# Optimization experiments

Hardware: AMD Instinct MI355X
Metric: run time of the kernel (lower is better)

The kernel has to match this reference:

```python
import jax, jax.numpy as jnp
import numpy as np

B = 131072      # batch of states
STATE = 32      # state dim
HIDDEN = 256    # MLP hidden width
NOUT = 32       # MLP outputs (summed after relu -> scalar value)
ACT = 8         # action dim (QP size)
QP_ITERS = 30   # BoxCDQP coordinate-descent sweeps


def setup_inputs() -> dict:
    key = jax.random.key(0)
    ks = jax.random.split(key, 8)
    sc = lambda fan: 1.0 / np.sqrt(fan)
    x = jax.random.normal(ks[0], (B, STATE), jnp.float32)
    t = jnp.zeros((1,), jnp.float32)
    W0 = jax.random.normal(ks[1], (STATE, HIDDEN), jnp.float32) * sc(STATE)
    b0 = jnp.zeros((HIDDEN,), jnp.float32)
    W1 = jax.random.normal(ks[2], (HIDDEN, HIDDEN), jnp.float32) * sc(HIDDEN)
    b1 = jnp.zeros((HIDDEN,), jnp.float32)
    W2 = jax.random.normal(ks[3], (HIDDEN, HIDDEN), jnp.float32) * sc(HIDDEN)
    b2 = jnp.zeros((HIDDEN,), jnp.float32)
    Wout = jax.random.normal(ks[4], (HIDDEN, NOUT), jnp.float32) * sc(HIDDEN)
    bout = jnp.zeros((NOUT,), jnp.float32)
    G = jax.random.normal(ks[5], (STATE, ACT), jnp.float32) * sc(STATE)
    A = jax.random.normal(ks[6], (ACT, ACT), jnp.float32)
    R = A @ A.T / ACT + jnp.eye(ACT, dtype=jnp.float32)  # symmetric PD cost
    lower = -jnp.ones((ACT,), jnp.float32)
    upper = jnp.ones((ACT,), jnp.float32)
    return dict(x=x, t=t, W0=W0, b0=b0, W1=W1, b1=b1, W2=W2, b2=b2,
                Wout=Wout, bout=bout, G=G, R=R, lower=lower, upper=upper)


def _v(xi, W0, b0, W1, b1, W2, b2, Wout, bout):
    # v(x) = sum(relu(MLP(angle_rep(x)))), angle_rep = identity here
    h = jax.nn.softplus(xi @ W0 + b0)
    h = jax.nn.softplus(h @ W1 + b1)
    h = jax.nn.softplus(h @ W2 + b2)
    return jnp.sum(jax.nn.relu(h @ Wout + bout))


def _box_cdqp(Q, c, lo, hi):
    # BoxCDQP: min 0.5 u^T Q u + c^T u  s.t. lo <= u <= hi, cyclic coord descent
    diag = jnp.diag(Q)

    def sweep(u, _):
        for i in range(ACT):  # ACT is small and static -> unrolled
            gi = Q[i] @ u + c[i]
            u = u.at[i].set(jnp.clip(u[i] - gi / diag[i], lo[i], hi[i]))
        return u, None

    u, _ = jax.lax.scan(sweep, jnp.zeros_like(c), None, length=QP_ITERS)
    return u


def reference(x, t, W0, b0, W1, b1, W2, b2, Wout, bout, G, R, lower, upper):
    # dv/dx per sample via grad of scalar v, batched with vmap
    dvdx = jax.vmap(
        lambda xi: jax.grad(_v)(xi, W0, b0, W1, b1, W2, b2, Wout, bout)
    )(x)                                  # [B, STATE]
    c = dvdx @ G                          # [B, ACT] linear QP term (dvdx @ gx)
    Q = 2.0 * R                           # params_obj = (2*R, dvdx_gx)
    u = jax.vmap(lambda ci: _box_cdqp(Q, ci, lower, upper))(c)  # [B, ACT]
    return u
```

## Files before the change

kernel.cpp:

```cpp
#include <hip/hip_runtime.h>
#include <math.h>

typedef float f4 __attribute__((ext_vector_type(4)));

#define THREADS 256
#define HID 256
#define SMP 16
#define CH 16

__global__ void k_prep(const float* __restrict__ W1, const float* __restrict__ W2,
                       const float* __restrict__ Wout, float* __restrict__ ws) {
  float* W1T = ws;
  float* W2T = ws + 65536;
  float* WoutT = ws + 131072;
  int tid = blockIdx.x * 256 + threadIdx.x;
  if (tid < 65536) {
    int k = tid >> 8, n = tid & 255;
    W1T[tid] = W1[n * 256 + k];
    W2T[tid] = W2[n * 256 + k];
    if (tid < 8192) {
      int k2 = tid >> 8, n2 = tid & 255;
      WoutT[tid] = Wout[n2 * 32 + k2];
    }
  }
}

__device__ __forceinline__ float sp_cr(float z) {
  float az = fabsf(z);
  float e  = (float)exp(-(double)az);
  float lp = (float)log1p((double)e);
  return fmaxf(z, 0.0f) + lp;
}

__device__ __forceinline__ float sig_from_h(float h) {
  return 1.0f - __expf(-h);
}

__device__ __forceinline__ void mac_fwd4(const float* __restrict__ h0r,
                                         const float* __restrict__ h1r,
                                         const float* __restrict__ h2r,
                                         const float* __restrict__ h3r,
                                         const float* __restrict__ wl,
                                         int l, f4& a0, f4& a1, f4& a2, f4& a3) {
#pragma clang fp contract(off)
  #pragma unroll
  for (int k = 0; k < CH; k += 4) {
    f4 x0 = *(const f4*)&h0r[k];
    f4 x1 = *(const f4*)&h1r[k];
    f4 x2 = *(const f4*)&h2r[k];
    f4 x3 = *(const f4*)&h3r[k];
    #pragma unroll
    for (int kk = 0; kk < 4; ++kk) {
      f4 wv = *(const f4*)&wl[(k + kk) * 256 + l * 4];
      #pragma unroll
      for (int m = 0; m < 4; ++m) { float p = x0[kk] * wv[m]; a0[m] = a0[m] + p; }
      #pragma unroll
      for (int m = 0; m < 4; ++m) { float p = x1[kk] * wv[m]; a1[m] = a1[m] + p; }
      #pragma unroll
      for (int m = 0; m < 4; ++m) { float p = x2[kk] * wv[m]; a2[m] = a2[m] + p; }
      #pragma unroll
      for (int m = 0; m < 4; ++m) { float p = x3[kk] * wv[m]; a3[m] = a3[m] + p; }
    }
  }
}

__device__ __forceinline__ void mac_bwd4(const float* __restrict__ h0r,
                                         const float* __restrict__ h1r,
                                         const float* __restrict__ h2r,
                                         const float* __restrict__ h3r,
                                         const float* __restrict__ wl,
                                         int l, f4& a0, f4& a1, f4& a2, f4& a3) {
  #pragma unroll
  for (int k = 0; k < CH; k += 4) {
    f4 x0 = *(const f4*)&h0r[k];
    f4 x1 = *(const f4*)&h1r[k];
    f4 x2 = *(const f4*)&h2r[k];
    f4 x3 = *(const f4*)&h3r[k];
    #pragma unroll
    for (int kk = 0; kk < 4; ++kk) {
      f4 wv = *(const f4*)&wl[(k + kk) * 256 + l * 4];
      #pragma unroll
      for (int m = 0; m < 4; ++m) a0[m] = fmaf(x0[kk], wv[m], a0[m]);
      #pragma unroll
      for (int m = 0; m < 4; ++m) a1[m] = fmaf(x1[kk], wv[m], a1[m]);
      #pragma unroll
      for (int m = 0; m < 4; ++m) a2[m] = fmaf(x2[kk], wv[m], a2[m]);
      #pragma unroll
      for (int m = 0; m < 4; ++m) a3[m] = fmaf(x3[kk], wv[m], a3[m]);
    }
  }
}

template <int K, bool FWD>
__device__ __forceinline__ void staged_layer(
    const float* __restrict__ Wbase,
    const float* __restrict__ hin,
    int sA, int l, int tid, f4* wbuf4, const float* wl,
    f4& a0, f4& a1, f4& a2, f4& a3) {
  a0 = (f4){0, 0, 0, 0}; a1 = a0; a2 = a0; a3 = a0;
  const f4* src = (const f4*)Wbase;
  f4 r0 = src[tid];
  f4 r1 = src[tid + THREADS];
  f4 r2 = src[tid + 2 * THREADS];
  f4 r3 = src[tid + 3 * THREADS];
  constexpr int NC = K / CH;
  #pragma unroll 1
  for (int c = 0; c < NC; ++c) {
    __syncthreads();
    wbuf4[tid] = r0;
    wbuf4[tid + THREADS] = r1;
    wbuf4[tid + 2 * THREADS] = r2;
    wbuf4[tid + 3 * THREADS] = r3;
    __syncthreads();
    if (c + 1 < NC) {
      const f4* s2 = (const f4*)(Wbase + (size_t)(c + 1) * CH * 256);
      r0 = s2[tid];
      r1 = s2[tid + THREADS];
      r2 = s2[tid + 2 * THREADS];
      r3 = s2[tid + 3 * THREADS];
    }
    const float* h0 = hin + (size_t)(sA + 0) * K + c * CH;
    const float* h1 = hin + (size_t)(sA + 1) * K + c * CH;
    const float* h2 = hin + (size_t)(sA + 2) * K + c * CH;
    const float* h3 = hin + (size_t)(sA + 3) * K + c * CH;
    if constexpr (FWD) mac_fwd4(h0, h1, h2, h3, wl, l, a0, a1, a2, a3);
    else               mac_bwd4(h0, h1, h2, h3, wl, l, a0, a1, a2, a3);
  }
}

__device__ __forceinline__ void sp_store(f4 a, const float* __restrict__ b,
                                         float* __restrict__ dstrow, int l) {
  f4 bv = *(const f4*)&b[l * 4];
  f4 o;
  #pragma unroll
  for (int m = 0; m < 4; ++m) o[m] = sp_cr(a[m] + bv[m]);
  *(f4*)&dstrow[l * 4] = o;
}

__device__ __forceinline__ void sig_store(f4 a, float* __restrict__ hrow, int l) {
  f4 h = *(f4*)&hrow[l * 4];
  #pragma unroll
  for (int m = 0; m < 4; ++m) h[m] = a[m] * sig_from_h(h[m]);
  *(f4*)&hrow[l * 4] = h;
}

__global__ __launch_bounds__(THREADS, 2) void k_main(
    const float* __restrict__ x,
    const float* __restrict__ W0, const float* __restrict__ b0,
    const float* __restrict__ W1, const float* __restrict__ b1,
    const float* __restrict__ W2, const float* __restrict__ b2,
    const float* __restrict__ Wout, const float* __restrict__ bout,
    const float* __restrict__ G, const float* __restrict__ ws,
    float* __restrict__ out) {
  __shared__ float xs[SMP][32];
  __shared__ float ha[SMP][HID];
  __shared__ float hb[SMP][HID];
  __shared__ float hc[SMP][HID];
  __shared__ float zm[SMP][32];
  __shared__ f4 wbuf4[CH * 64];
  float* wl = (float*)wbuf4;

  const float* W1T = ws;
  const float* W2T = ws + 65536;
  const float* WoutT = ws + 131072;

  const int tid = threadIdx.x;
  const int w = tid >> 6;
  const int l = tid & 63;
  const int sA = w * 4;
  const int s0 = blockIdx.x * SMP;

  for (int i = tid; i < SMP * 32; i += THREADS) {
    xs[i >> 5][i & 31] = x[(size_t)s0 * 32 + i];
  }

  {
    f4 a0, a1, a2, a3;
    staged_layer<32, true>(W0, &xs[0][0], sA, l, tid, wbuf4, wl, a0, a1, a2, a3);
    sp_store(a0, b0, &ha[sA + 0][0], l);
    sp_store(a1, b0, &ha[sA + 1][0], l);
    sp_store(a2, b0, &ha[sA + 2][0], l);
    sp_store(a3, b0, &ha[sA + 3][0], l);
  }

  {
    f4 a0, a1, a2, a3;
    staged_layer<256, true>(W1, &ha[0][0], sA, l, tid, wbuf4, wl, a0, a1, a2, a3);
    sp_store(a0, b1, &hb[sA + 0][0], l);
    sp_store(a1, b1, &hb[sA + 1][0], l);
    sp_store(a2, b1, &hb[sA + 2][0], l);
    sp_store(a3, b1, &hb[sA + 3][0], l);
  }

  {
    f4 a0, a1, a2, a3;
    staged_layer<256, true>(W2, &hb[0][0], sA, l, tid, wbuf4, wl, a0, a1, a2, a3);
    sp_store(a0, b2, &hc[sA + 0][0], l);
    sp_store(a1, b2, &hc[sA + 1][0], l);
    sp_store(a2, b2, &hc[sA + 2][0], l);
    sp_store(a3, b2, &hc[sA + 3][0], l);
  }
  __syncthreads();

  {
#pragma clang fp contract(off)
    #pragma unroll
    for (int rep = 0; rep < 2; ++rep) {
      int idx = tid + rep * THREADS;
      int s = idx >> 5, j = idx & 31;
      const float* wrow = WoutT + (size_t)j * 256;
      float acc = 0.0f;
      #pragma unroll 4
      for (int k = 0; k < 256; k += 4) {
        f4 hv = *(const f4*)&hc[s][k];
        f4 wv = *(const f4*)&wrow[k];
        #pragma unroll
        for (int kk = 0; kk < 4; ++kk) {
          float p = hv[kk] * wv[kk];
          acc = acc + p;
        }
      }
      zm[s][j] = (acc + bout[j] > 0.0f) ? 1.0f : 0.0f;
    }
  }

  {
    f4 a0, a1, a2, a3;
    staged_layer<32, false>(WoutT, &zm[0][0], sA, l, tid, wbuf4, wl, a0, a1, a2, a3);
    sig_store(a0, &hc[sA + 0][0], l);
    sig_store(a1, &hc[sA + 1][0], l);
    sig_store(a2, &hc[sA + 2][0], l);
    sig_store(a3, &hc[sA + 3][0], l);
  }

  {
    f4 a0, a1, a2, a3;
    staged_layer<256, false>(W2T, &hc[0][0], sA, l, tid, wbuf4, wl, a0, a1, a2, a3);
    sig_store(a0, &hb[sA + 0][0], l);
    sig_store(a1, &hb[sA + 1][0], l);
    sig_store(a2, &hb[sA + 2][0], l);
    sig_store(a3, &hb[sA + 3][0], l);
  }

  {
    f4 a0, a1, a2, a3;
    staged_layer<256, false>(W1T, &hb[0][0], sA, l, tid, wbuf4, wl, a0, a1, a2, a3);
    sig_store(a0, &ha[sA + 0][0], l);
    sig_store(a1, &ha[sA + 1][0], l);
    sig_store(a2, &ha[sA + 2][0], l);
    sig_store(a3, &ha[sA + 3][0], l);
  }
  __syncthreads();

  {
    #pragma unroll
    for (int rep = 0; rep < 2; ++rep) {
      int idx = tid + rep * THREADS;
      int s = idx >> 5, j = idx & 31;
      const float* wrow = W0 + (size_t)j * 256;
      float acc = 0.0f;
      #pragma unroll 4
      for (int k = 0; k < 256; k += 4) {
        f4 hv = *(const f4*)&ha[s][k];
        f4 wv = *(const f4*)&wrow[k];
        #pragma unroll
        for (int kk = 0; kk < 4; ++kk) {
          acc = fmaf(hv[kk], wv[kk], acc);
        }
      }
      zm[s][j] = acc;
    }
  }
  __syncthreads();

  if (tid < SMP * 8) {
    int s = tid >> 3, a = tid & 7;
    float acc = 0.0f;
    #pragma unroll
    for (int j = 0; j < 32; ++j) acc = fmaf(zm[s][j], G[j * 8 + a], acc);
    out[(size_t)(s0 + s) * 8 + a] = acc;
  }
}

__global__ __launch_bounds__(256) void k_qp(float* __restrict__ out,
                                            const float* __restrict__ R,
                                            const float* __restrict__ lower,
                                            const float* __restrict__ upper) {
  int t = blockIdx.x * 256 + threadIdx.x;
  float q[8][8], u[8], cc[8], lo[8], hi[8], dg[8];
  #pragma unroll
  for (int i = 0; i < 8; ++i) {
    lo[i] = lower[i];
    hi[i] = upper[i];
    u[i] = 0.0f;
    cc[i] = out[(size_t)t * 8 + i];
    #pragma unroll
    for (int j = 0; j < 8; ++j) q[i][j] = 2.0f * R[i * 8 + j];
  }
  #pragma unroll
  for (int i = 0; i < 8; ++i) dg[i] = q[i][i];

  #pragma unroll 1
  for (int it = 0; it < 30; ++it) {
    #pragma unroll
    for (int i = 0; i < 8; ++i) {
      float g = cc[i];
      #pragma unroll
      for (int j = 0; j < 8; ++j) g = fmaf(q[i][j], u[j], g);
      float v = u[i] - g / dg[i];
      u[i] = fminf(fmaxf(v, lo[i]), hi[i]);
    }
  }
  #pragma unroll
  for (int i = 0; i < 8; ++i) out[(size_t)t * 8 + i] = u[i];
}

extern "C" void kernel_launch(void* const* d_in, const int* in_sizes, int n_in,
                              void* d_out, int out_size, void* d_ws, size_t ws_size,
                              hipStream_t stream) {
  const float* x    = (const float*)d_in[0];
  const float* W0   = (const float*)d_in[2];
  const float* b0   = (const float*)d_in[3];
  const float* W1   = (const float*)d_in[4];
  const float* b1   = (const float*)d_in[5];
  const float* W2   = (const float*)d_in[6];
  const float* b2   = (const float*)d_in[7];
  const float* Wout = (const float*)d_in[8];
  const float* bout = (const float*)d_in[9];
  const float* G    = (const float*)d_in[10];
  const float* R    = (const float*)d_in[11];
  const float* lower= (const float*)d_in[12];
  const float* upper= (const float*)d_in[13];
  float* out = (float*)d_out;
  float* ws  = (float*)d_ws;

  const int B = in_sizes[0] / 32;

  k_prep<<<256, 256, 0, stream>>>(W1, W2, Wout, ws);
  k_main<<<B / SMP, THREADS, 0, stream>>>(x, W0, b0, W1, b1, W2, b2,
                                          Wout, bout, G, ws, out);
  k_qp<<<B / 256, 256, 0, stream>>>(out, R, lower, upper);
}
```

Measured before the change: 2.011 ms.

## Keep layer activations in registers and broadcast via readlane instead of LDS reads

Each wave already owns 4 samples with 4 hidden columns per lane, so the 256-wide hidden layers now feed the next layer straight from registers. Each input element is broadcast to the wave with readlane instead of being reread from shared memory. This removes LDS loads of activation rows from the inner multiply loops of the W1, W2 and backward layers. The cost is four scalar readlane operations per k step in place of vector LDS loads, which may add SALU/VALU serialization and register pressure.

```diff
diff --git a/kernel.cpp b/kernel.cpp
--- a/kernel.cpp
+++ b/kernel.cpp
@@ -36,12 +36,16 @@
   return 1.0f - __expf(-h);
 }
 
-__device__ __forceinline__ void mac_fwd4(const float* __restrict__ h0r,
-                                         const float* __restrict__ h1r,
-                                         const float* __restrict__ h2r,
-                                         const float* __restrict__ h3r,
-                                         const float* __restrict__ wl,
-                                         int l, f4& a0, f4& a1, f4& a2, f4& a3) {
+__device__ __forceinline__ float bcast(float v, int ln) {
+  return __uint_as_float(__builtin_amdgcn_readlane(__float_as_uint(v), ln));
+}
+
+__device__ __forceinline__ void mac_fwd(const float* __restrict__ h0r,
+                                        const float* __restrict__ h1r,
+                                        const float* __restrict__ h2r,
+                                        const float* __restrict__ h3r,
+                                        const float* __restrict__ wl,
+                                        int l, f4& a0, f4& a1, f4& a2, f4& a3) {
 #pragma clang fp contract(off)
   #pragma unroll
   for (int k = 0; k < CH; k += 4) {
@@ -64,12 +68,12 @@
   }
 }
 
-__device__ __forceinline__ void mac_bwd4(const float* __restrict__ h0r,
-                                         const float* __restrict__ h1r,
-                                         const float* __restrict__ h2r,
-                                         const float* __restrict__ h3r,
-                                         const float* __restrict__ wl,
-                                         int l, f4& a0, f4& a1, f4& a2, f4& a3) {
+__device__ __forceinline__ void mac_bwd(const float* __restrict__ h0r,
+                                        const float* __restrict__ h1r,
+                                        const float* __restrict__ h2r,
+                                        const float* __restrict__ h3r,
+                                        const float* __restrict__ wl,
+                                        int l, f4& a0, f4& a1, f4& a2, f4& a3) {
   #pragma unroll
   for (int k = 0; k < CH; k += 4) {
     f4 x0 = *(const f4*)&h0r[k];
@@ -91,10 +95,11 @@
   }
 }
 
-template <int K, bool FWD>
-__device__ __forceinline__ void staged_layer(
+template <int K, bool FWD, bool REG>
+__device__ __forceinline__ void layer(
     const float* __restrict__ Wbase,
     const float* __restrict__ hin,
+    f4 d0, f4 d1, f4 d2, f4 d3,
     int sA, int l, int tid, f4* wbuf4, const float* wl,
     f4& a0, f4& a1, f4& a2, f4& a3) {
   a0 = (f4){0, 0, 0, 0}; a1 = a0; a2 = a0; a3 = a0;
@@ -119,22 +124,72 @@
       r2 = s2[tid + 2 * THREADS];
       r3 = s2[tid + 3 * THREADS];
     }
-    const float* h0 = hin + (size_t)(sA + 0) * K + c * CH;
-    const float* h1 = hin + (size_t)(sA + 1) * K + c * CH;
-    const float* h2 = hin + (size_t)(sA + 2) * K + c * CH;
-    const float* h3 = hin + (size_t)(sA + 3) * K + c * CH;
-    if constexpr (FWD) mac_fwd4(h0, h1, h2, h3, wl, l, a0, a1, a2, a3);
-    else               mac_bwd4(h0, h1, h2, h3, wl, l, a0, a1, a2, a3);
-  }
-}
-
-__device__ __forceinline__ void sp_store(f4 a, const float* __restrict__ b,
-                                         float* __restrict__ dstrow, int l) {
+    if constexpr (REG) {
+      if constexpr (FWD) {
+#pragma clang fp contract(off)
+        #pragma unroll
+        for (int kk = 0; kk < CH; ++kk) {
+          f4 wv = *(const f4*)&wl[kk * 256 + l * 4];
+          int ln = c * 4 + (kk >> 2);
+          float b0v = bcast(d0[kk & 3], ln);
+          float b1v = bcast(d1[kk & 3], ln);
+          float b2v = bcast(d2[kk & 3], ln);
+          float b3v = bcast(d3[kk & 3], ln);
+          #pragma unroll
+          for (int m = 0; m < 4; ++m) { float p = b0v * wv[m]; a0[m] = a0[m] + p; }
+          #pragma unroll
+          for (int m = 0; m < 4; ++m) { float p = b1v * wv[m]; a1[m] = a1[m] + p; }
+          #pragma unroll
+          for (int m = 0; m < 4; ++m) { float p = b2v * wv[m]; a2[m] = a2[m] + p; }
+          #pragma unroll
+          for (int m = 0; m < 4; ++m) { float p = b3v * wv[m]; a3[m] = a3[m] + p; }
+        }
+      } else {
+        #pragma unroll
+        for (int kk = 0; kk < CH; ++kk) {
+          f4 wv = *(const f4*)&wl[kk * 256 + l * 4];
+          int ln = c * 4 + (kk >> 2);
+          float b0v = bcast(d0[kk & 3], ln);
+          float b1v = bcast(d1[kk & 3], ln);
+          float b2v = bcast(d2[kk & 3], ln);
+          float b3v = bcast(d3[kk & 3], ln);
+          #pragma unroll
+          for (int m = 0; m < 4; ++m) a0[m] = fmaf(b0v, wv[m], a0[m]);
+          #pragma unroll
+          for (int m = 0; m < 4; ++m) a1[m] = fmaf(b1v, wv[m], a1[m]);
+          #pragma unroll
+          for (int m = 0; m < 4; ++m) a2[m] = fmaf(b2v, wv[m], a2[m]);
+          #pragma unroll
+          for (int m = 0; m < 4; ++m) a3[m] = fmaf(b3v, wv[m], a3[m]);
+        }
+      }
+    } else {
+      const float* h0 = hin + (size_t)(sA + 0) * K + c * CH;
+      const float* h1 = hin + (size_t)(sA + 1) * K + c * CH;
+      const float* h2 = hin + (size_t)(sA + 2) * K + c * CH;
+      const float* h3 = hin + (size_t)(sA + 3) * K + c * CH;
+      if constexpr (FWD) mac_fwd(h0, h1, h2, h3, wl, l, a0, a1, a2, a3);
+      else               mac_bwd(h0, h1, h2, h3, wl, l, a0, a1, a2, a3);
+    }
+  }
+}
+
+__device__ __forceinline__ f4 sp_rs(f4 a, const float* __restrict__ b,
+                                    float* __restrict__ dstrow, int l) {
   f4 bv = *(const f4*)&b[l * 4];
   f4 o;
   #pragma unroll
   for (int m = 0; m < 4; ++m) o[m] = sp_cr(a[m] + bv[m]);
   *(f4*)&dstrow[l * 4] = o;
+  return o;
+}
+
+__device__ __forceinline__ f4 sig_ret(f4 a, const float* __restrict__ hrow, int l) {
+  f4 h = *(const f4*)&hrow[l * 4];
+  f4 d;
+  #pragma unroll
+  for (int m = 0; m < 4; ++m) d[m] = a[m] * sig_from_h(h[m]);
+  return d;
 }
 
 __device__ __forceinline__ void sig_store(f4 a, float* __restrict__ hrow, int l) {
@@ -174,32 +229,30 @@
     xs[i >> 5][i & 31] = x[(size_t)s0 * 32 + i];
   }
 
-  {
-    f4 a0, a1, a2, a3;
-    staged_layer<32, true>(W0, &xs[0][0], sA, l, tid, wbuf4, wl, a0, a1, a2, a3);
-    sp_store(a0, b0, &ha[sA + 0][0], l);
-    sp_store(a1, b0, &ha[sA + 1][0], l);
-    sp_store(a2, b0, &ha[sA + 2][0], l);
-    sp_store(a3, b0, &ha[sA + 3][0], l);
-  }
-
-  {
-    f4 a0, a1, a2, a3;
-    staged_layer<256, true>(W1, &ha[0][0], sA, l, tid, wbuf4, wl, a0, a1, a2, a3);
-    sp_store(a0, b1, &hb[sA + 0][0], l);
-    sp_store(a1, b1, &hb[sA + 1][0], l);
-    sp_store(a2, b1, &hb[sA + 2][0], l);
-    sp_store(a3, b1, &hb[sA + 3][0], l);
-  }
-
-  {
-    f4 a0, a1, a2, a3;
-    staged_layer<256, true>(W2, &hb[0][0], sA, l, tid, wbuf4, wl, a0, a1, a2, a3);
-    sp_store(a0, b2, &hc[sA + 0][0], l);
-    sp_store(a1, b2, &hc[sA + 1][0], l);
-    sp_store(a2, b2, &hc[sA + 2][0], l);
-    sp_store(a3, b2, &hc[sA + 3][0], l);
-  }
+  f4 a0, a1, a2, a3;
+  f4 o0, o1, o2, o3;
+  f4 zz = {0, 0, 0, 0};
+
+  layer<32, true, false>(W0, &xs[0][0], zz, zz, zz, zz, sA, l, tid, wbuf4, wl,
+                         a0, a1, a2, a3);
+  o0 = sp_rs(a0, b0, &ha[sA + 0][0], l);
+  o1 = sp_rs(a1, b0, &ha[sA + 1][0], l);
+  o2 = sp_rs(a2, b0, &ha[sA + 2][0], l);
+  o3 = sp_rs(a3, b0, &ha[sA + 3][0], l);
+
+  layer<256, true, true>(W1, nullptr, o0, o1, o2, o3, sA, l, tid, wbuf4, wl,
+                         a0, a1, a2, a3);
+  o0 = sp_rs(a0, b1, &hb[sA + 0][0], l);
+  o1 = sp_rs(a1, b1, &hb[sA + 1][0], l);
+  o2 = sp_rs(a2, b1, &hb[sA + 2][0], l);
+  o3 = sp_rs(a3, b1, &hb[sA + 3][0], l);
+
+  layer<256, true, true>(W2, nullptr, o0, o1, o2, o3, sA, l, tid, wbuf4, wl,
+                         a0, a1, a2, a3);
+  o0 = sp_rs(a0, b2, &hc[sA + 0][0], l);
+  o1 = sp_rs(a1, b2, &hc[sA + 1][0], l);
+  o2 = sp_rs(a2, b2, &hc[sA + 2][0], l);
+  o3 = sp_rs(a3, b2, &hc[sA + 3][0], l);
   __syncthreads();
 
   {
@@ -224,32 +277,26 @@
     }
   }
 
-  {
-    f4 a0, a1, a2, a3;
-    staged_layer<32, false>(WoutT, &zm[0][0], sA, l, tid, wbuf4, wl, a0, a1, a2, a3);
-    sig_store(a0, &hc[sA + 0][0], l);
-    sig_store(a1, &hc[sA + 1][0], l);
-    sig_store(a2, &hc[sA + 2][0], l);
-    sig_store(a3, &hc[sA + 3][0], l);
-  }
-
-  {
-    f4 a0, a1, a2, a3;
-    staged_layer<256, false>(W2T, &hc[0][0], sA, l, tid, wbuf4, wl, a0, a1, a2, a3);
-    sig_store(a0, &hb[sA + 0][0], l);
-    sig_store(a1, &hb[sA + 1][0], l);
-    sig_store(a2, &hb[sA + 2][0], l);
-    sig_store(a3, &hb[sA + 3][0], l);
-  }
-
-  {
-    f4 a0, a1, a2, a3;
-    staged_layer<256, false>(W1T, &hb[0][0], sA, l, tid, wbuf4, wl, a0, a1, a2, a3);
-    sig_store(a0, &ha[sA + 0][0], l);
-    sig_store(a1, &ha[sA + 1][0], l);
-    sig_store(a2, &ha[sA + 2][0], l);
-    sig_store(a3, &ha[sA + 3][0], l);
-  }
+  layer<32, false, false>(WoutT, &zm[0][0], zz, zz, zz, zz, sA, l, tid, wbuf4,
+                          wl, a0, a1, a2, a3);
+  f4 d0 = sig_ret(a0, &hc[sA + 0][0], l);
+  f4 d1 = sig_ret(a1, &hc[sA + 1][0], l);
+  f4 d2 = sig_ret(a2, &hc[sA + 2][0], l);
+  f4 d3 = sig_ret(a3, &hc[sA + 3][0], l);
+
+  layer<256, false, true>(W2T, nullptr, d0, d1, d2, d3, sA, l, tid, wbuf4, wl,
+                          a0, a1, a2, a3);
+  d0 = sig_ret(a0, &hb[sA + 0][0], l);
+  d1 = sig_ret(a1, &hb[sA + 1][0], l);
+  d2 = sig_ret(a2, &hb[sA + 2][0], l);
+  d3 = sig_ret(a3, &hb[sA + 3][0], l);
+
+  layer<256, false, true>(W1T, nullptr, d0, d1, d2, d3, sA, l, tid, wbuf4, wl,
+                          a0, a1, a2, a3);
+  sig_store(a0, &ha[sA + 0][0], l);
+  sig_store(a1, &ha[sA + 1][0], l);
+  sig_store(a2, &ha[sA + 2][0], l);
+  sig_store(a3, &ha[sA + 3][0], l);
   __syncthreads();
 
   {
```

After: 2.227 ms. 1.11x slower.
